# Performance work log

Measured on AMD Instinct MI355X. Metric: run time of the kernel, lower is better.

## Reference

```python
import jax, jax.numpy as jnp
import numpy as np

# Model dims (from init_kwargs): T=12, dx=4, du=2 -> D = T*(dx+du) = 72
T, DX, DU = 12, 4, 2
D = T * (DX + DU)          # flow_dim = 72
MID = D // 2               # mid-split mask: first MID features transformed
CTX = 2 * DX               # context = cat(start, goal) = 8
HID = 64                   # ResidualNet / MLP hidden size
NBLK = 16                  # number of (LULinear, Coupling) blocks
B = 65536


def setup_inputs() -> dict:
    key = jax.random.key(0)
    ks = jax.random.split(key, 16)
    n = lambda k, s, sc=1.0: sc * jax.random.normal(k, s, dtype=jnp.float32)
    inp = {
        "trajectories": n(ks[0], (B, T, DX + DU)),
        "start": n(ks[1], (B, DX)),
        "goal": n(ks[2], (B, DX)),
        # LULinear params per block: strictly-lower / strictly-upper entries,
        # unconstrained diag (softplus(0.5413)~=1 -> near-identity init), bias
        "lu_lower": n(ks[3], (NBLK, D, D), 0.01),
        "lu_upper": n(ks[4], (NBLK, D, D), 0.01),
        "lu_diag": 0.5413 + n(ks[5], (NBLK, D), 0.01),
        "lu_bias": n(ks[6], (NBLK, D), 0.01),
        # Coupling conditioner ResidualNet (in=MID+CTX, hidden=64, 2 blocks, out=2*MID)
        "cn_W0": n(ks[7], (NBLK, HID, MID + CTX), 0.05),
        "cn_b0": jnp.zeros((NBLK, HID), jnp.float32),
        "cn_ctxW": n(ks[8], (NBLK, 2, HID, CTX), 0.1),
        "cn_ctxb": jnp.zeros((NBLK, 2, HID), jnp.float32),
        "cn_l1W": n(ks[9], (NBLK, 2, HID, HID), 0.1),
        "cn_l1b": jnp.zeros((NBLK, 2, HID), jnp.float32),
        "cn_l2W": n(ks[10], (NBLK, 2, HID, HID), 0.1),
        "cn_l2b": jnp.zeros((NBLK, 2, HID), jnp.float32),
        "cn_Wf": n(ks[11], (NBLK, D, HID), 0.05),
        "cn_bf": jnp.zeros((NBLK, D), jnp.float32),
        # ConditionalDiagonalNormal context encoder MLP: ctx -> 2*D
        "enc_W1": n(ks[12], (HID, CTX), 0.1),
        "enc_b1": jnp.zeros((HID,), jnp.float32),
        "enc_W2": n(ks[13], (2 * D, HID), 0.05),
        "enc_b2": jnp.zeros((2 * D,), jnp.float32),
    }
    return inp


def reference(trajectories, start, goal, lu_lower, lu_upper, lu_diag, lu_bias,
              cn_W0, cn_b0, cn_ctxW, cn_ctxb, cn_l1W, cn_l1b, cn_l2W, cn_l2b,
              cn_Wf, cn_bf, enc_W1, enc_b1, enc_W2, enc_b2):
    Bn = trajectories.shape[0]
    x = trajectories.reshape(Bn, D)
    ctx = jnp.concatenate([start, goal], axis=1)  # [B, CTX]
    eye = jnp.eye(D, dtype=x.dtype)

    def resnet(h, W0, b0, cW, cb, l1W, l1b, l2W, l2b, Wf, bf):
        # nflows ResidualNet: initial layer on cat(inputs, context), 2 residual
        # blocks with GLU context gating, final linear.
        t = jnp.concatenate([h, ctx], axis=1) @ W0.T + b0
        for i in range(2):
            a = jax.nn.relu(t) @ l1W[i].T + l1b[i]
            a = jax.nn.relu(a) @ l2W[i].T + l2b[i]
            t = t + a * jax.nn.sigmoid(ctx @ cW[i].T + cb[i])  # GLU
        return t @ Wf.T + bf

    def body(carry, p):
        x, ld = carry
        lL, lU, ldg, lb, W0, b0, cW, cb, l1W, l1b, l2W, l2b, Wf, bf = p
        # LULinear: W = L @ U, L unit lower-tri, U upper-tri, diag = softplus + eps
        diag = jax.nn.softplus(ldg) + 1e-3
        W = (jnp.tril(lL, -1) + eye) @ (jnp.triu(lU, 1) + jnp.diag(diag))
        x = x @ W.T + lb
        ld = ld + jnp.sum(jnp.log(diag))
        # Affine coupling, mid-split: first MID transformed, last MID identity
        h_id = x[:, MID:]
        params = resnet(h_id, W0, b0, cW, cb, l1W, l1b, l2W, l2b, Wf, bf)
        shift = params[:, :MID]
        scale = jax.nn.sigmoid(params[:, MID:] + 2.0) + 1e-3
        x = jnp.concatenate([x[:, :MID] * scale + shift, h_id], axis=1)
        ld = ld + jnp.sum(jnp.log(scale), axis=1)
        return (x, ld), None

    stacked = (lu_lower, lu_upper, lu_diag, lu_bias, cn_W0, cn_b0, cn_ctxW,
               cn_ctxb, cn_l1W, cn_l1b, cn_l2W, cn_l2b, cn_Wf, cn_bf)
    (noise, logdet), _ = jax.lax.scan(body, (x, jnp.zeros((Bn,), x.dtype)), stacked)

    # ConditionalDiagonalNormal base: encoder MLP ctx -> (means, log_stds)
    h = jax.nn.relu(ctx @ enc_W1.T + enc_b1)
    p = h @ enc_W2.T + enc_b2
    means, log_std = p[:, :D], p[:, D:]
    z = (noise - means) * jnp.exp(-log_std)
    base_lp = (-0.5 * jnp.sum(z * z, axis=1) - jnp.sum(log_std, axis=1)
               - 0.5 * D * jnp.log(2.0 * jnp.pi))
    return base_lp + logdet
```

## Files before the change

### kernel.cpp

```cpp
#include <hip/hip_runtime.h>
#include <math.h>

#define DD   72
#define MID  36
#define NBLK 16

typedef _Float16 half8 __attribute__((ext_vector_type(8)));
typedef _Float16 half4 __attribute__((ext_vector_type(4)));
typedef float    f32x4 __attribute__((ext_vector_type(4)));

#define PB    37376
#define S1O   0
#define S2O   7680
#define RBO   11776
#define RB_L1 0
#define RB_L2 4096
#define RB_GW 8192
#define S4O   32256
#define E1O   (16 * PB)
#define E2O   (E1O + 2048)
#define AR_TOTAL (E2O + 18 * 512)

__device__ inline half4 pk4(f32x4 v) {
    half4 h; h[0] = (_Float16)v[0]; h[1] = (_Float16)v[1];
    h[2] = (_Float16)v[2]; h[3] = (_Float16)v[3]; return h;
}
__device__ inline half4 pk4r(f32x4 v) {
    half4 h;
    h[0] = (_Float16)fmaxf(v[0], 0.f); h[1] = (_Float16)fmaxf(v[1], 0.f);
    h[2] = (_Float16)fmaxf(v[2], 0.f); h[3] = (_Float16)fmaxf(v[3], 0.f);
    return h;
}
__device__ inline float sigf(float x) {
    return __fdividef(1.f, 1.f + __expf(-x));
}

__global__ __launch_bounds__(256) void prep_lu(
    const float* __restrict__ lu_lower,
    const float* __restrict__ lu_upper,
    const float* __restrict__ lu_diag,
    const float* __restrict__ lu_bias,
    _Float16* __restrict__ AR, float* __restrict__ wsLd)
{
    const int wg  = blockIdx.x;
    const int blk = wg / 5, mt = wg % 5;
    const int tid = threadIdx.x;
    __shared__ float Ls[DD][DD + 1];
    __shared__ float Us[DD][DD + 1];
    __shared__ float diag[DD], ldp[DD];

    const float* L = lu_lower + blk * DD * DD;
    const float* U = lu_upper + blk * DD * DD;
    for (int e = tid; e < DD * DD; e += 256) {
        Ls[e / DD][e % DD] = L[e];
        Us[e / DD][e % DD] = U[e];
    }
    if (tid < DD) {
        float v  = lu_diag[blk * DD + tid];
        float sp = log1pf(expf(v)) + 0.001f;
        diag[tid] = sp; ldp[tid] = logf(sp);
    }
    __syncthreads();
    if (mt == 0 && tid == 0) {
        float s = 0.f;
        for (int i = 0; i < DD; ++i) s += ldp[i];
        wsLd[blk] = s;
    }

    if (tid < 192) {
        const int kt   = tid >> 6, lane = tid & 63;
        const int m    = mt * 16 + (lane & 15);
        const int k0   = kt * 32 + (lane >> 4) * 8;
        float acc[8] = {0.f, 0.f, 0.f, 0.f, 0.f, 0.f, 0.f, 0.f};
        if (m < DD) {
            for (int kk = 0; kk < m; ++kk) {
                const float a = Ls[m][kk];
                #pragma unroll
                for (int j = 0; j < 8; ++j) {
                    const int k = k0 + j;
                    if (k < DD && kk < k) acc[j] = fmaf(a, Us[kk][k], acc[j]);
                }
            }
            #pragma unroll
            for (int j = 0; j < 8; ++j) {
                const int k = k0 + j;
                if (k < DD) {
                    if      (m < k)  acc[j] += Us[m][k];
                    else if (m == k) acc[j] += diag[k];
                    else             acc[j] += Ls[m][k] * diag[k];
                }
            }
        }
        half8 hv;
        #pragma unroll
        for (int j = 0; j < 8; ++j) {
            const int k = k0 + j;
            float v = 0.f;
            if (m < DD) {
                if      (k < DD)  v = acc[j];
                else if (k == DD) v = lu_bias[blk * DD + m];
            }
            hv[j] = (_Float16)v;
        }
        *(half8*)(AR + (size_t)blk * PB + S1O + (size_t)(mt * 3 + kt) * 512
                  + (size_t)lane * 8) = hv;
    }
}

__global__ __launch_bounds__(256) void prep_w(
    const float* __restrict__ cn_W0, const float* __restrict__ cn_ctxW,
    const float* __restrict__ cn_l1W, const float* __restrict__ cn_l2W,
    const float* __restrict__ cn_Wf, const float* __restrict__ enc_W1,
    const float* __restrict__ enc_W2,
    const float* __restrict__ cn_b0, const float* __restrict__ cn_ctxb,
    const float* __restrict__ enc_b1,
    _Float16* __restrict__ AR)
{
    int gid = blockIdx.x * 256 + threadIdx.x;
    int fid = gid >> 6, lane = gid & 63;
    if (fid >= 950) return;
    const int mrow = lane & 15, kcol0 = (lane >> 4) * 8;

    const float* src = nullptr; const float* bias = nullptr;
    size_t dst = 0;
    int m = 0, kbase = 0, rows = 64, kv_lo = 0, kv_hi = 64, sstr = 64, ksub = 0, kbias = -1;

    if (fid < 128) {
        int blk = fid >> 3, f = fid & 7;
        int mt = f >> 1, kt = f & 1;
        src = cn_W0 + (size_t)blk * 64 * 44; sstr = 44;
        dst = (size_t)blk * PB + S2O + (size_t)f * 512;
        m = mt * 16 + mrow; kbase = kt * 32 + kcol0; kv_hi = 44;
        bias = cn_b0 + (size_t)blk * 64; kbias = 44;
    } else if (fid < 384) {
        int id = fid - 128, bi = id >> 3, f = id & 7;
        int mt = f >> 1, kt = f & 1;
        src = cn_l1W + (size_t)bi * 4096;
        dst = (size_t)(bi >> 1) * PB + RBO + (size_t)(bi & 1) * 10240 + RB_L1 + (size_t)f * 512;
        m = mt * 16 + mrow; kbase = kt * 32 + kcol0;
    } else if (fid < 640) {
        int id = fid - 384, bi = id >> 3, f = id & 7;
        int mt = f >> 1, kt = f & 1;
        src = cn_l2W + (size_t)bi * 4096;
        dst = (size_t)(bi >> 1) * PB + RBO + (size_t)(bi & 1) * 10240 + RB_L2 + (size_t)f * 512;
        m = mt * 16 + mrow; kbase = kt * 32 + kcol0;
    } else if (fid < 768) {
        int id = fid - 640, bi = id >> 2, mt = id & 3;
        src = cn_ctxW + (size_t)bi * 512; sstr = 8;
        dst = (size_t)(bi >> 1) * PB + RBO + (size_t)(bi & 1) * 10240 + RB_GW + (size_t)mt * 512;
        m = mt * 16 + mrow; kbase = 32 + kcol0; kv_lo = 36; kv_hi = 44; ksub = 36;
        bias = cn_ctxb + (size_t)bi * 64; kbias = 44;
    } else if (fid < 928) {
        int id = fid - 768, blk = id / 10, f = id % 10;
        int mt = f >> 1, kt = f & 1;
        src = cn_Wf + (size_t)blk * 4608;
        dst = (size_t)blk * PB + S4O + (size_t)f * 512;
        m = mt * 16 + mrow; kbase = kt * 32 + kcol0; rows = 72;
    } else if (fid < 932) {
        int mt = fid - 928;
        src = enc_W1; sstr = 8;
        dst = E1O + (size_t)mt * 512;
        m = mt * 16 + mrow; kbase = 32 + kcol0; kv_lo = 36; kv_hi = 44; ksub = 36;
        bias = enc_b1; kbias = 44;
    } else {
        int id = fid - 932, mt = id >> 1, kt = id & 1;
        src = enc_W2;
        dst = E2O + (size_t)id * 512;
        m = mt * 16 + mrow; kbase = kt * 32 + kcol0; rows = 144;
    }
    half8 hv;
    #pragma unroll
    for (int j = 0; j < 8; ++j) {
        const int k = kbase + j;
        float v = 0.f;
        if (m < rows) {
            if (k >= kv_lo && k < kv_hi) v = src[(size_t)m * sstr + (k - ksub)];
            else if (k == kbias)         v = bias[m];
        }
        hv[j] = (_Float16)v;
    }
    *(half8*)(AR + dst + (size_t)lane * 8) = hv;
}

#define MFMA_A(acc, off, bf) \
    acc = __builtin_amdgcn_mfma_f32_16x16x32_f16( \
        *(const half8*)(AR + (size_t)(off) + (size_t)lane * 8), bf, acc, 0, 0, 0)

__global__ __launch_bounds__(256, 4) void flow_kernel(
    const float* __restrict__ traj,
    const float* __restrict__ start,
    const float* __restrict__ goal,
    const float* __restrict__ cn_l1b,
    const float* __restrict__ cn_l2b,
    const float* __restrict__ cn_bf,
    const float* __restrict__ enc_b2,
    const _Float16* __restrict__ AR,
    const float* __restrict__ wsLd,
    float* __restrict__ out, int B)
{
    __shared__ __align__(16) _Float16 ActX[64 * 104];
    __shared__ __align__(16) _Float16 ActH[64 * 72];
    __shared__ __align__(16) _Float16 ActT[64 * 72];

    const int tid  = threadIdx.x;
    const int lane = tid & 63;
    const int w    = __builtin_amdgcn_readfirstlane(tid >> 6);
    const int n    = lane & 15, lg = lane >> 4;
    const int bg0  = blockIdx.x * 64;

    #pragma unroll
    for (int r = 0; r < 9; ++r) {
        int e = tid + 256 * r;
        int b = e / 36, p = e % 36;
        float2 v = *(const float2*)(traj + (size_t)(bg0 + b) * DD + 2 * p);
        ActX[b * 104 + 2 * p]     = (_Float16)v.x;
        ActX[b * 104 + 2 * p + 1] = (_Float16)v.y;
    }
    #pragma unroll
    for (int r = 0; r < 8; ++r) {
        int e = tid + 256 * r;
        int b = e / 32, c = 72 + e % 32;
        ActX[b * 104 + c] = (c == 72) ? (_Float16)1.f : (_Float16)0.f;
    }
    {
        int b = tid >> 2, cp = tid & 3;
        const float* s = (cp < 2) ? (start + (size_t)(bg0 + b) * 4 + 2 * cp)
                                  : (goal  + (size_t)(bg0 + b) * 4 + 2 * (cp - 2));
        ActH[b * 72 + 36 + 2 * cp]     = (_Float16)s[0];
        ActH[b * 72 + 36 + 2 * cp + 1] = (_Float16)s[1];
    }
    #pragma unroll
    for (int r = 0; r < 7; ++r) {
        int e = tid + 256 * r;
        int b = e / 28, c = 44 + e % 28;
        ActH[b * 72 + c] = (c == 44) ? (_Float16)1.f : (_Float16)0.f;
    }
    __syncthreads();

    const int bx = (16 * w + n) * 104;
    const int bh = (16 * w + n) * 72;
    const int bt = (16 * w + n) * 72;

    float ld_acc = 0.f;
    const f32x4 z4 = {0.f, 0.f, 0.f, 0.f};

    #pragma unroll 1
    for (int blk = 0; blk < NBLK; ++blk) {
        __syncthreads();
        const size_t B0 = (size_t)blk * PB;

        half8 bx0 = *(const half8*)&ActX[bx + 0  + lg * 8];
        half8 bx1 = *(const half8*)&ActX[bx + 32 + lg * 8];
        half8 bx2 = *(const half8*)&ActX[bx + 64 + lg * 8];
        f32x4 y[5];
        #pragma unroll
        for (int mt = 0; mt < 5; ++mt) {
            f32x4 a = z4;
            MFMA_A(a, B0 + S1O + (mt * 3 + 0) * 512, bx0);
            MFMA_A(a, B0 + S1O + (mt * 3 + 1) * 512, bx1);
            MFMA_A(a, B0 + S1O + (mt * 3 + 2) * 512, bx2);
            y[mt] = a;
        }
        if (lg >= 1) { half4 hv = pk4(y[2]); int m0 = 32 + lg * 4;
            *(half4*)&ActX[bx + m0] = hv; *(half4*)&ActH[bh + m0 - 36] = hv; }
        {            half4 hv = pk4(y[3]); int m0 = 48 + lg * 4;
            *(half4*)&ActX[bx + m0] = hv; *(half4*)&ActH[bh + m0 - 36] = hv; }
        if (lg < 2) { half4 hv = pk4(y[4]); int m0 = 64 + lg * 4;
            *(half4*)&ActX[bx + m0] = hv; *(half4*)&ActH[bh + m0 - 36] = hv; }

        half8 bh0 = *(const half8*)&ActH[bh + 0  + lg * 8];
        half8 bh1 = *(const half8*)&ActH[bh + 32 + lg * 8];
        f32x4 t[4];
        #pragma unroll
        for (int mt = 0; mt < 4; ++mt) {
            f32x4 a = z4;
            MFMA_A(a, B0 + S2O + (mt * 2 + 0) * 512, bh0);
            MFMA_A(a, B0 + S2O + (mt * 2 + 1) * 512, bh1);
            t[mt] = a;
        }

        #pragma unroll 1
        for (int i = 0; i < 2; ++i) {
            const size_t RB = B0 + RBO + (size_t)i * 10240;
            #pragma unroll
            for (int mt = 0; mt < 4; ++mt)
                *(half4*)&ActT[bt + mt * 16 + lg * 4] = pk4r(t[mt]);
            half8 bt0 = *(const half8*)&ActT[bt + 0  + lg * 8];
            half8 bt1 = *(const half8*)&ActT[bt + 32 + lg * 8];
            f32x4 a1[4];
            #pragma unroll
            for (int mt = 0; mt < 4; ++mt) {
                f32x4 a = z4;
                MFMA_A(a, RB + RB_L1 + (mt * 2 + 0) * 512, bt0);
                MFMA_A(a, RB + RB_L1 + (mt * 2 + 1) * 512, bt1);
                const float4 bb = *(const float4*)(cn_l1b + (blk * 2 + i) * 64 + mt * 16 + lg * 4);
                a1[mt][0] = a[0] + bb.x; a1[mt][1] = a[1] + bb.y;
                a1[mt][2] = a[2] + bb.z; a1[mt][3] = a[3] + bb.w;
            }
            #pragma unroll
            for (int mt = 0; mt < 4; ++mt)
                *(half4*)&ActT[bt + mt * 16 + lg * 4] = pk4r(a1[mt]);
            bt0 = *(const half8*)&ActT[bt + 0  + lg * 8];
            bt1 = *(const half8*)&ActT[bt + 32 + lg * 8];
            #pragma unroll
            for (int mt = 0; mt < 4; ++mt) {
                f32x4 a = z4;
                MFMA_A(a, RB + RB_L2 + (mt * 2 + 0) * 512, bt0);
                MFMA_A(a, RB + RB_L2 + (mt * 2 + 1) * 512, bt1);
                const float4 b2 = *(const float4*)(cn_l2b + (blk * 2 + i) * 64 + mt * 16 + lg * 4);
                f32x4 g = z4;
                MFMA_A(g, RB + RB_GW + mt * 512, bh1);
                #pragma unroll
                for (int r = 0; r < 4; ++r) {
                    float a2 = a[r] + ((const float*)&b2)[r];
                    float gg = sigf(g[r]);
                    t[mt][r] = fmaf(a2, gg, t[mt][r]);
                }
            }
        }

        #pragma unroll
        for (int mt = 0; mt < 4; ++mt)
            *(half4*)&ActT[bt + mt * 16 + lg * 4] = pk4(t[mt]);
        half8 bt0 = *(const half8*)&ActT[bt + 0  + lg * 8];
        half8 bt1 = *(const half8*)&ActT[bt + 32 + lg * 8];
        f32x4 p[5];
        #pragma unroll
        for (int mt = 0; mt < 5; ++mt) {
            f32x4 a = z4;
            MFMA_A(a, B0 + S4O + (mt * 2 + 0) * 512, bt0);
            MFMA_A(a, B0 + S4O + (mt * 2 + 1) * 512, bt1);
            int bm = mt * 16 + lg * 4; if (bm > 68) bm = 68;
            const float4 bb = *(const float4*)(cn_bf + blk * DD + bm);
            p[mt][0] = a[0] + bb.x; p[mt][1] = a[1] + bb.y;
            p[mt][2] = a[2] + bb.z; p[mt][3] = a[3] + bb.w;
        }
        if (lg >= 1) {
            f32x4 s;
            #pragma unroll
            for (int r = 0; r < 4; ++r) {
                s[r] = sigf(p[2][r] + 2.f) + 0.001f;
                ld_acc += __logf(s[r]);
            }
            *(half4*)&ActT[bt + (32 + lg * 4) - 36] = pk4(s);
        }
        {
            f32x4 s;
            #pragma unroll
            for (int r = 0; r < 4; ++r) {
                s[r] = sigf(p[3][r] + 2.f) + 0.001f;
                ld_acc += __logf(s[r]);
            }
            *(half4*)&ActT[bt + (48 + lg * 4) - 36] = pk4(s);
        }
        if (lg < 2) {
            f32x4 s;
            #pragma unroll
            for (int r = 0; r < 4; ++r) {
                s[r] = sigf(p[4][r] + 2.f) + 0.001f;
                ld_acc += __logf(s[r]);
            }
            *(half4*)&ActT[bt + (64 + lg * 4) - 36] = pk4(s);
        }
        {
            half4 sv = *(const half4*)&ActT[bt + lg * 4];
            f32x4 xn;
            #pragma unroll
            for (int r = 0; r < 4; ++r) xn[r] = fmaf(y[0][r], (float)sv[r], p[0][r]);
            *(half4*)&ActX[bx + lg * 4] = pk4(xn);
        }
        {
            half4 sv = *(const half4*)&ActT[bt + 16 + lg * 4];
            f32x4 xn;
            #pragma unroll
            for (int r = 0; r < 4; ++r) xn[r] = fmaf(y[1][r], (float)sv[r], p[1][r]);
            *(half4*)&ActX[bx + 16 + lg * 4] = pk4(xn);
        }
        if (lg == 0) {
            half4 sv = *(const half4*)&ActT[bt + 32];
            f32x4 xn;
            #pragma unroll
            for (int r = 0; r < 4; ++r) xn[r] = fmaf(y[2][r], (float)sv[r], p[2][r]);
            *(half4*)&ActX[bx + 32] = pk4(xn);
        }
    }

    half8 bh1 = *(const half8*)&ActH[bh + 32 + lg * 8];
    #pragma unroll
    for (int mt = 0; mt < 4; ++mt) {
        f32x4 a = z4;
        MFMA_A(a, E1O + mt * 512, bh1);
        *(half4*)&ActT[bt + mt * 16 + lg * 4] = pk4r(a);
    }
    half8 bt0 = *(const half8*)&ActT[bt + 0  + lg * 8];
    half8 bt1 = *(const half8*)&ActT[bt + 32 + lg * 8];
    f32x4 me[9];
    #pragma unroll
    for (int mt = 0; mt < 9; ++mt) {
        f32x4 a = z4;
        MFMA_A(a, E2O + (mt * 2 + 0) * 512, bt0);
        MFMA_A(a, E2O + (mt * 2 + 1) * 512, bt1);
        const float4 bb = *(const float4*)(enc_b2 + mt * 16 + lg * 4);
        me[mt][0] = a[0] + bb.x; me[mt][1] = a[1] + bb.y;
        me[mt][2] = a[2] + bb.z; me[mt][3] = a[3] + bb.w;
    }
    float slsp = 0.f, qp = 0.f;
    if (lg >= 2) {
        #pragma unroll
        for (int r = 0; r < 4; ++r) slsp += me[4][r];
        *(half4*)&ActT[bt + lg * 4 - 8] = pk4(me[4]);
    }
    #pragma unroll
    for (int mt = 5; mt < 9; ++mt) {
        #pragma unroll
        for (int r = 0; r < 4; ++r) slsp += me[mt][r];
        *(half4*)&ActT[bt + (mt * 16 + lg * 4) - 72] = pk4(me[mt]);
    }
    #pragma unroll
    for (int mt = 0; mt < 4; ++mt) {
        int m0 = mt * 16 + lg * 4;
        half4 xv = *(const half4*)&ActX[bx + m0];
        half4 lv = *(const half4*)&ActT[bt + m0];
        #pragma unroll
        for (int r = 0; r < 4; ++r) {
            float zz = ((float)xv[r] - me[mt][r]) * __expf(-(float)lv[r]);
            qp = fmaf(zz, zz, qp);
        }
    }
    if (lg < 2) {
        int m0 = 64 + lg * 4;
        half4 xv = *(const half4*)&ActX[bx + m0];
        half4 lv = *(const half4*)&ActT[bt + m0];
        #pragma unroll
        for (int r = 0; r < 4; ++r) {
            float zz = ((float)xv[r] - me[4][r]) * __expf(-(float)lv[r]);
            qp = fmaf(zz, zz, qp);
        }
    }

    qp     += __shfl_xor(qp, 16);     qp     += __shfl_xor(qp, 32);
    slsp   += __shfl_xor(slsp, 16);   slsp   += __shfl_xor(slsp, 32);
    ld_acc += __shfl_xor(ld_acc, 16); ld_acc += __shfl_xor(ld_acc, 32);
    if (lane < 16) {
        float ldsum = 0.f;
        #pragma unroll
        for (int k = 0; k < NBLK; ++k) ldsum += wsLd[k];
        out[bg0 + 16 * w + lane] = -0.5f * qp - slsp - 66.1635744f + ld_acc + ldsum;
    }
}

extern "C" void kernel_launch(void* const* d_in, const int* in_sizes, int n_in,
                              void* d_out, int out_size, void* d_ws, size_t ws_size,
                              hipStream_t stream) {
    const float* traj     = (const float*)d_in[0];
    const float* start    = (const float*)d_in[1];
    const float* goal     = (const float*)d_in[2];
    const float* lu_lower = (const float*)d_in[3];
    const float* lu_upper = (const float*)d_in[4];
    const float* lu_diag  = (const float*)d_in[5];
    const float* lu_bias  = (const float*)d_in[6];
    const float* cn_W0    = (const float*)d_in[7];
    const float* cn_b0    = (const float*)d_in[8];
    const float* cn_ctxW  = (const float*)d_in[9];
    const float* cn_ctxb  = (const float*)d_in[10];
    const float* cn_l1W   = (const float*)d_in[11];
    const float* cn_l1b   = (const float*)d_in[12];
    const float* cn_l2W   = (const float*)d_in[13];
    const float* cn_l2b   = (const float*)d_in[14];
    const float* cn_Wf    = (const float*)d_in[15];
    const float* cn_bf    = (const float*)d_in[16];
    const float* enc_W1   = (const float*)d_in[17];
    const float* enc_b1   = (const float*)d_in[18];
    const float* enc_W2   = (const float*)d_in[19];
    const float* enc_b2   = (const float*)d_in[20];

    float* outp = (float*)d_out;
    const int B = in_sizes[0] / DD;

    float*     wsLd = (float*)d_ws;
    _Float16*  AR   = (_Float16*)((char*)d_ws + 256);

    hipLaunchKernelGGL(prep_lu, dim3(NBLK * 5), dim3(256), 0, stream,
                       lu_lower, lu_upper, lu_diag, lu_bias, AR, wsLd);
    hipLaunchKernelGGL(prep_w, dim3((950 * 64 + 255) / 256), dim3(256), 0, stream,
                       cn_W0, cn_ctxW, cn_l1W, cn_l2W, cn_Wf, enc_W1, enc_W2,
                       cn_b0, cn_ctxb, enc_b1, AR);

    hipLaunchKernelGGL(flow_kernel, dim3(B / 64), dim3(256), 0, stream,
                       traj, start, goal,
                       cn_l1b, cn_l2b, cn_bf, enc_b2,
                       AR, wsLd, outp, B);
}
```

Baseline: 388.5 us.

## Batch weight fragment loads ahead of MFMAs, prefetch next block, merge prep kernels

The flow kernel now loads each stage's weight fragments from global memory into registers as a batch before the MFMA chain that uses them, instead of loading inside each MFMA call. The first LU fragments for the next block are prefetched at the end of the current block, and the residual loop is fully unrolled. This hides global-load latency behind compute. The two prep kernels are also merged into one launch to save launch overhead. The cost is much higher register pressure, which at launch_bounds(256,4) may cause spills or lower occupancy.

Measured after the change: 354.3 us. 1.1x faster.

```diff
diff --git a/kernel.cpp b/kernel.cpp
--- a/kernel.cpp
+++ b/kernel.cpp
@@ -19,7 +19,6 @@
 #define S4O   32256
 #define E1O   (16 * PB)
 #define E2O   (E1O + 2048)
-#define AR_TOTAL (E2O + 18 * 512)
 
 __device__ inline half4 pk4(f32x4 v) {
     half4 h; h[0] = (_Float16)v[0]; h[1] = (_Float16)v[1];
@@ -34,89 +33,88 @@
 __device__ inline float sigf(float x) {
     return __fdividef(1.f, 1.f + __expf(-x));
 }
-
-__global__ __launch_bounds__(256) void prep_lu(
-    const float* __restrict__ lu_lower,
-    const float* __restrict__ lu_upper,
-    const float* __restrict__ lu_diag,
-    const float* __restrict__ lu_bias,
-    _Float16* __restrict__ AR, float* __restrict__ wsLd)
-{
-    const int wg  = blockIdx.x;
-    const int blk = wg / 5, mt = wg % 5;
-    const int tid = threadIdx.x;
-    __shared__ float Ls[DD][DD + 1];
-    __shared__ float Us[DD][DD + 1];
-    __shared__ float diag[DD], ldp[DD];
-
-    const float* L = lu_lower + blk * DD * DD;
-    const float* U = lu_upper + blk * DD * DD;
-    for (int e = tid; e < DD * DD; e += 256) {
-        Ls[e / DD][e % DD] = L[e];
-        Us[e / DD][e % DD] = U[e];
-    }
-    if (tid < DD) {
-        float v  = lu_diag[blk * DD + tid];
-        float sp = log1pf(expf(v)) + 0.001f;
-        diag[tid] = sp; ldp[tid] = logf(sp);
-    }
-    __syncthreads();
-    if (mt == 0 && tid == 0) {
-        float s = 0.f;
-        for (int i = 0; i < DD; ++i) s += ldp[i];
-        wsLd[blk] = s;
-    }
-
-    if (tid < 192) {
-        const int kt   = tid >> 6, lane = tid & 63;
-        const int m    = mt * 16 + (lane & 15);
-        const int k0   = kt * 32 + (lane >> 4) * 8;
-        float acc[8] = {0.f, 0.f, 0.f, 0.f, 0.f, 0.f, 0.f, 0.f};
-        if (m < DD) {
-            for (int kk = 0; kk < m; ++kk) {
-                const float a = Ls[m][kk];
-                #pragma unroll
-                for (int j = 0; j < 8; ++j) {
-                    const int k = k0 + j;
-                    if (k < DD && kk < k) acc[j] = fmaf(a, Us[kk][k], acc[j]);
-                }
-            }
-            #pragma unroll
-            for (int j = 0; j < 8; ++j) {
-                const int k = k0 + j;
-                if (k < DD) {
-                    if      (m < k)  acc[j] += Us[m][k];
-                    else if (m == k) acc[j] += diag[k];
-                    else             acc[j] += Ls[m][k] * diag[k];
-                }
-            }
-        }
-        half8 hv;
-        #pragma unroll
-        for (int j = 0; j < 8; ++j) {
-            const int k = k0 + j;
-            float v = 0.f;
-            if (m < DD) {
-                if      (k < DD)  v = acc[j];
-                else if (k == DD) v = lu_bias[blk * DD + m];
-            }
-            hv[j] = (_Float16)v;
-        }
-        *(half8*)(AR + (size_t)blk * PB + S1O + (size_t)(mt * 3 + kt) * 512
-                  + (size_t)lane * 8) = hv;
-    }
-}
-
-__global__ __launch_bounds__(256) void prep_w(
+__device__ inline f32x4 MF(half8 a, half8 b, f32x4 c) {
+    return __builtin_amdgcn_mfma_f32_16x16x32_f16(a, b, c, 0, 0, 0);
+}
+
+__global__ __launch_bounds__(256) void prep_all(
+    const float* __restrict__ lu_lower, const float* __restrict__ lu_upper,
+    const float* __restrict__ lu_diag,  const float* __restrict__ lu_bias,
     const float* __restrict__ cn_W0, const float* __restrict__ cn_ctxW,
     const float* __restrict__ cn_l1W, const float* __restrict__ cn_l2W,
     const float* __restrict__ cn_Wf, const float* __restrict__ enc_W1,
     const float* __restrict__ enc_W2,
     const float* __restrict__ cn_b0, const float* __restrict__ cn_ctxb,
     const float* __restrict__ enc_b1,
-    _Float16* __restrict__ AR)
+    _Float16* __restrict__ AR, float* __restrict__ wsLd)
 {
-    int gid = blockIdx.x * 256 + threadIdx.x;
+    const int tid = threadIdx.x;
+    __shared__ float Ls[DD][DD + 1];
+    __shared__ float Us[DD][DD + 1];
+    __shared__ float diag[DD], ldp[DD];
+
+    if (blockIdx.x < 80) {
+        const int wg  = blockIdx.x;
+        const int blk = wg / 5, mt = wg % 5;
+        const float* L = lu_lower + blk * DD * DD;
+        const float* U = lu_upper + blk * DD * DD;
+        for (int e = tid; e < DD * DD; e += 256) {
+            Ls[e / DD][e % DD] = L[e];
+            Us[e / DD][e % DD] = U[e];
+        }
+        if (tid < DD) {
+            float v  = lu_diag[blk * DD + tid];
+            float sp = log1pf(expf(v)) + 0.001f;
+            diag[tid] = sp; ldp[tid] = logf(sp);
+        }
+        __syncthreads();
+        if (mt == 0 && tid == 0) {
+            float s = 0.f;
+            for (int i = 0; i < DD; ++i) s += ldp[i];
+            wsLd[blk] = s;
+        }
+        if (tid < 192) {
+            const int kt = tid >> 6, lane = tid & 63;
+            const int m  = mt * 16 + (lane & 15);
+            const int k0 = kt * 32 + (lane >> 4) * 8;
+            float acc[8] = {0.f,0.f,0.f,0.f,0.f,0.f,0.f,0.f};
+            if (m < DD) {
+                for (int kk = 0; kk < m; ++kk) {
+                    const float a = Ls[m][kk];
+                    #pragma unroll
+                    for (int j = 0; j < 8; ++j) {
+                        const int k = k0 + j;
+                        if (k < DD && kk < k) acc[j] = fmaf(a, Us[kk][k], acc[j]);
+                    }
+                }
+                #pragma unroll
+                for (int j = 0; j < 8; ++j) {
+                    const int k = k0 + j;
+                    if (k < DD) {
+                        if      (m < k)  acc[j] += Us[m][k];
+                        else if (m == k) acc[j] += diag[k];
+                        else             acc[j] += Ls[m][k] * diag[k];
+                    }
+                }
+            }
+            half8 hv;
+            #pragma unroll
+            for (int j = 0; j < 8; ++j) {
+                const int k = k0 + j;
+                float v = 0.f;
+                if (m < DD) {
+                    if      (k < DD)  v = acc[j];
+                    else if (k == DD) v = lu_bias[blk * DD + m];
+                }
+                hv[j] = (_Float16)v;
+            }
+            *(half8*)(AR + (size_t)blk * PB + S1O + (size_t)(mt * 3 + kt) * 512
+                      + (size_t)lane * 8) = hv;
+        }
+        return;
+    }
+
+    int gid = (blockIdx.x - 80) * 256 + tid;
     int fid = gid >> 6, lane = gid & 63;
     if (fid >= 950) return;
     const int mrow = lane & 15, kcol0 = (lane >> 4) * 8;
@@ -182,9 +180,8 @@
     *(half8*)(AR + dst + (size_t)lane * 8) = hv;
 }
 
-#define MFMA_A(acc, off, bf) \
-    acc = __builtin_amdgcn_mfma_f32_16x16x32_f16( \
-        *(const half8*)(AR + (size_t)(off) + (size_t)lane * 8), bf, acc, 0, 0, 0)
+#define LDH8(off) (*(const half8*)(AR + (size_t)(off) + lane8))
+#define MFMA_A(acc, off, bf) acc = MF(LDH8(off), bf, acc)
 
 __global__ __launch_bounds__(256, 4) void flow_kernel(
     const float* __restrict__ traj,
@@ -207,6 +204,7 @@
     const int w    = __builtin_amdgcn_readfirstlane(tid >> 6);
     const int n    = lane & 15, lg = lane >> 4;
     const int bg0  = blockIdx.x * 64;
+    const size_t lane8 = (size_t)lane * 8;
 
     #pragma unroll
     for (int r = 0; r < 9; ++r) {
@@ -235,6 +233,11 @@
         int b = e / 28, c = 44 + e % 28;
         ActH[b * 72 + c] = (c == 44) ? (_Float16)1.f : (_Float16)0.f;
     }
+
+    half8 s1p0 = LDH8(S1O + 0 * 512), s1p1 = LDH8(S1O + 1 * 512),
+          s1p2 = LDH8(S1O + 2 * 512), s1p3 = LDH8(S1O + 3 * 512),
+          s1p4 = LDH8(S1O + 4 * 512), s1p5 = LDH8(S1O + 5 * 512);
+
     __syncthreads();
 
     const int bx = (16 * w + n) * 104;
@@ -249,92 +252,118 @@
         __syncthreads();
         const size_t B0 = (size_t)blk * PB;
 
+        half8 f6  = LDH8(B0 + S1O + 6 * 512),  f7  = LDH8(B0 + S1O + 7 * 512),
+              f8  = LDH8(B0 + S1O + 8 * 512),  f9  = LDH8(B0 + S1O + 9 * 512),
+              f10 = LDH8(B0 + S1O + 10 * 512), f11 = LDH8(B0 + S1O + 11 * 512),
+              f12 = LDH8(B0 + S1O + 12 * 512), f13 = LDH8(B0 + S1O + 13 * 512),
+              f14 = LDH8(B0 + S1O + 14 * 512);
         half8 bx0 = *(const half8*)&ActX[bx + 0  + lg * 8];
         half8 bx1 = *(const half8*)&ActX[bx + 32 + lg * 8];
         half8 bx2 = *(const half8*)&ActX[bx + 64 + lg * 8];
         f32x4 y[5];
-        #pragma unroll
-        for (int mt = 0; mt < 5; ++mt) {
-            f32x4 a = z4;
-            MFMA_A(a, B0 + S1O + (mt * 3 + 0) * 512, bx0);
-            MFMA_A(a, B0 + S1O + (mt * 3 + 1) * 512, bx1);
-            MFMA_A(a, B0 + S1O + (mt * 3 + 2) * 512, bx2);
-            y[mt] = a;
-        }
+        y[0] = MF(s1p2, bx2, MF(s1p1, bx1, MF(s1p0, bx0, z4)));
+        y[1] = MF(s1p5, bx2, MF(s1p4, bx1, MF(s1p3, bx0, z4)));
+        y[2] = MF(f8,  bx2, MF(f7,  bx1, MF(f6,  bx0, z4)));
+        y[3] = MF(f11, bx2, MF(f10, bx1, MF(f9,  bx0, z4)));
+        y[4] = MF(f14, bx2, MF(f13, bx1, MF(f12, bx0, z4)));
+
+        half8 g0 = LDH8(B0 + S2O + 0 * 512), g1 = LDH8(B0 + S2O + 1 * 512),
+              g2 = LDH8(B0 + S2O + 2 * 512), g3 = LDH8(B0 + S2O + 3 * 512),
+              g4 = LDH8(B0 + S2O + 4 * 512), g5 = LDH8(B0 + S2O + 5 * 512),
+              g6 = LDH8(B0 + S2O + 6 * 512), g7 = LDH8(B0 + S2O + 7 * 512);
         if (lg >= 1) { half4 hv = pk4(y[2]); int m0 = 32 + lg * 4;
             *(half4*)&ActX[bx + m0] = hv; *(half4*)&ActH[bh + m0 - 36] = hv; }
         {            half4 hv = pk4(y[3]); int m0 = 48 + lg * 4;
             *(half4*)&ActX[bx + m0] = hv; *(half4*)&ActH[bh + m0 - 36] = hv; }
         if (lg < 2) { half4 hv = pk4(y[4]); int m0 = 64 + lg * 4;
             *(half4*)&ActX[bx + m0] = hv; *(half4*)&ActH[bh + m0 - 36] = hv; }
-
         half8 bh0 = *(const half8*)&ActH[bh + 0  + lg * 8];
         half8 bh1 = *(const half8*)&ActH[bh + 32 + lg * 8];
         f32x4 t[4];
-        #pragma unroll
-        for (int mt = 0; mt < 4; ++mt) {
-            f32x4 a = z4;
-            MFMA_A(a, B0 + S2O + (mt * 2 + 0) * 512, bh0);
-            MFMA_A(a, B0 + S2O + (mt * 2 + 1) * 512, bh1);
-            t[mt] = a;
-        }
-
-        #pragma unroll 1
+        t[0] = MF(g1, bh1, MF(g0, bh0, z4));
+        t[1] = MF(g3, bh1, MF(g2, bh0, z4));
+        t[2] = MF(g5, bh1, MF(g4, bh0, z4));
+        t[3] = MF(g7, bh1, MF(g6, bh0, z4));
+
+        #pragma unroll
         for (int i = 0; i < 2; ++i) {
             const size_t RB = B0 + RBO + (size_t)i * 10240;
+            half8 r0 = LDH8(RB + RB_L1 + 0 * 512), r1 = LDH8(RB + RB_L1 + 1 * 512),
+                  r2 = LDH8(RB + RB_L1 + 2 * 512), r3 = LDH8(RB + RB_L1 + 3 * 512),
+                  r4 = LDH8(RB + RB_L1 + 4 * 512), r5 = LDH8(RB + RB_L1 + 5 * 512),
+                  r6 = LDH8(RB + RB_L1 + 6 * 512), r7 = LDH8(RB + RB_L1 + 7 * 512);
             #pragma unroll
             for (int mt = 0; mt < 4; ++mt)
                 *(half4*)&ActT[bt + mt * 16 + lg * 4] = pk4r(t[mt]);
             half8 bt0 = *(const half8*)&ActT[bt + 0  + lg * 8];
             half8 bt1 = *(const half8*)&ActT[bt + 32 + lg * 8];
             f32x4 a1[4];
+            a1[0] = MF(r1, bt1, MF(r0, bt0, z4));
+            a1[1] = MF(r3, bt1, MF(r2, bt0, z4));
+            a1[2] = MF(r5, bt1, MF(r4, bt0, z4));
+            a1[3] = MF(r7, bt1, MF(r6, bt0, z4));
+            half8 q0 = LDH8(RB + RB_L2 + 0 * 512), q1 = LDH8(RB + RB_L2 + 1 * 512),
+                  q2 = LDH8(RB + RB_L2 + 2 * 512), q3 = LDH8(RB + RB_L2 + 3 * 512),
+                  q4 = LDH8(RB + RB_L2 + 4 * 512), q5 = LDH8(RB + RB_L2 + 5 * 512),
+                  q6 = LDH8(RB + RB_L2 + 6 * 512), q7 = LDH8(RB + RB_L2 + 7 * 512);
+            half8 w0 = LDH8(RB + RB_GW + 0 * 512), w1 = LDH8(RB + RB_GW + 1 * 512),
+                  w2 = LDH8(RB + RB_GW + 2 * 512), w3 = LDH8(RB + RB_GW + 3 * 512);
             #pragma unroll
             for (int mt = 0; mt < 4; ++mt) {
-                f32x4 a = z4;
-                MFMA_A(a, RB + RB_L1 + (mt * 2 + 0) * 512, bt0);
-                MFMA_A(a, RB + RB_L1 + (mt * 2 + 1) * 512, bt1);
                 const float4 bb = *(const float4*)(cn_l1b + (blk * 2 + i) * 64 + mt * 16 + lg * 4);
-                a1[mt][0] = a[0] + bb.x; a1[mt][1] = a[1] + bb.y;
-                a1[mt][2] = a[2] + bb.z; a1[mt][3] = a[3] + bb.w;
-            }
-            #pragma unroll
-            for (int mt = 0; mt < 4; ++mt)
+                a1[mt][0] += bb.x; a1[mt][1] += bb.y; a1[mt][2] += bb.z; a1[mt][3] += bb.w;
                 *(half4*)&ActT[bt + mt * 16 + lg * 4] = pk4r(a1[mt]);
+            }
             bt0 = *(const half8*)&ActT[bt + 0  + lg * 8];
             bt1 = *(const half8*)&ActT[bt + 32 + lg * 8];
+            f32x4 a2[4], gg[4];
+            a2[0] = MF(q1, bt1, MF(q0, bt0, z4));
+            a2[1] = MF(q3, bt1, MF(q2, bt0, z4));
+            a2[2] = MF(q5, bt1, MF(q4, bt0, z4));
+            a2[3] = MF(q7, bt1, MF(q6, bt0, z4));
+            gg[0] = MF(w0, bh1, z4); gg[1] = MF(w1, bh1, z4);
+            gg[2] = MF(w2, bh1, z4); gg[3] = MF(w3, bh1, z4);
             #pragma unroll
             for (int mt = 0; mt < 4; ++mt) {
-                f32x4 a = z4;
-                MFMA_A(a, RB + RB_L2 + (mt * 2 + 0) * 512, bt0);
-                MFMA_A(a, RB + RB_L2 + (mt * 2 + 1) * 512, bt1);
                 const float4 b2 = *(const float4*)(cn_l2b + (blk * 2 + i) * 64 + mt * 16 + lg * 4);
-                f32x4 g = z4;
-                MFMA_A(g, RB + RB_GW + mt * 512, bh1);
                 #pragma unroll
                 for (int r = 0; r < 4; ++r) {
-                    float a2 = a[r] + ((const float*)&b2)[r];
-                    float gg = sigf(g[r]);
-                    t[mt][r] = fmaf(a2, gg, t[mt][r]);
+                    float av = a2[mt][r] + ((const float*)&b2)[r];
+                    t[mt][r] = fmaf(av, sigf(gg[mt][r]), t[mt][r]);
                 }
             }
         }
 
+        half8 h0 = LDH8(B0 + S4O + 0 * 512), h1 = LDH8(B0 + S4O + 1 * 512),
+              h2 = LDH8(B0 + S4O + 2 * 512), h3 = LDH8(B0 + S4O + 3 * 512),
+              h4 = LDH8(B0 + S4O + 4 * 512), h5 = LDH8(B0 + S4O + 5 * 512),
+              h6 = LDH8(B0 + S4O + 6 * 512), h7 = LDH8(B0 + S4O + 7 * 512),
+              h8 = LDH8(B0 + S4O + 8 * 512), h9 = LDH8(B0 + S4O + 9 * 512);
         #pragma unroll
         for (int mt = 0; mt < 4; ++mt)
             *(half4*)&ActT[bt + mt * 16 + lg * 4] = pk4(t[mt]);
         half8 bt0 = *(const half8*)&ActT[bt + 0  + lg * 8];
         half8 bt1 = *(const half8*)&ActT[bt + 32 + lg * 8];
         f32x4 p[5];
+        p[0] = MF(h1, bt1, MF(h0, bt0, z4));
+        p[1] = MF(h3, bt1, MF(h2, bt0, z4));
+        p[2] = MF(h5, bt1, MF(h4, bt0, z4));
+        p[3] = MF(h7, bt1, MF(h6, bt0, z4));
+        p[4] = MF(h9, bt1, MF(h8, bt0, z4));
         #pragma unroll
         for (int mt = 0; mt < 5; ++mt) {
-            f32x4 a = z4;
-            MFMA_A(a, B0 + S4O + (mt * 2 + 0) * 512, bt0);
-            MFMA_A(a, B0 + S4O + (mt * 2 + 1) * 512, bt1);
             int bm = mt * 16 + lg * 4; if (bm > 68) bm = 68;
             const float4 bb = *(const float4*)(cn_bf + blk * DD + bm);
-            p[mt][0] = a[0] + bb.x; p[mt][1] = a[1] + bb.y;
-            p[mt][2] = a[2] + bb.z; p[mt][3] = a[3] + bb.w;
-        }
+            p[mt][0] += bb.x; p[mt][1] += bb.y; p[mt][2] += bb.z; p[mt][3] += bb.w;
+        }
+
+        {
+            const size_t Bn = (size_t)(blk < NBLK - 1 ? blk + 1 : blk) * PB;
+            s1p0 = LDH8(Bn + S1O + 0 * 512); s1p1 = LDH8(Bn + S1O + 1 * 512);
+            s1p2 = LDH8(Bn + S1O + 2 * 512); s1p3 = LDH8(Bn + S1O + 3 * 512);
+            s1p4 = LDH8(Bn + S1O + 4 * 512); s1p5 = LDH8(Bn + S1O + 5 * 512);
+        }
+
         if (lg >= 1) {
             f32x4 s;
             #pragma unroll
@@ -480,11 +509,10 @@
     float*     wsLd = (float*)d_ws;
     _Float16*  AR   = (_Float16*)((char*)d_ws + 256);
 
-    hipLaunchKernelGGL(prep_lu, dim3(NBLK * 5), dim3(256), 0, stream,
-                       lu_lower, lu_upper, lu_diag, lu_bias, AR, wsLd);
-    hipLaunchKernelGGL(prep_w, dim3((950 * 64 + 255) / 256), dim3(256), 0, stream,
+    hipLaunchKernelGGL(prep_all, dim3(80 + 238), dim3(256), 0, stream,
+                       lu_lower, lu_upper, lu_diag, lu_bias,
                        cn_W0, cn_ctxW, cn_l1W, cn_l2W, cn_Wf, enc_W1, enc_W2,
-                       cn_b0, cn_ctxb, enc_b1, AR);
+                       cn_b0, cn_ctxb, enc_b1, AR, wsLd);
 
     hipLaunchKernelGGL(flow_kernel, dim3(B / 64), dim3(256), 0, stream,
                        traj, start, goal,
```
